# Kernel tuning notes

Hardware: AMD Instinct MI355X
Metric: run time of the kernel (lower is better)

## Reference

```python
import jax, jax.numpy as jnp
import numpy as np


def _update_cv(features, labels, ave, cov, amount, class_num):
    # Segment-reduce formulation of the onehot-expand update_CV.
    N, A = features.shape
    C = class_num
    counts = jax.ops.segment_sum(jnp.ones((N,), features.dtype), labels, num_segments=C)  # [C]
    sums = jax.ops.segment_sum(features, labels, num_segments=C)  # [C, A]
    denom = jnp.where(counts == 0, 1.0, counts)[:, None]  # Amount_CxA with zeros -> 1
    ave_CxA = sums / denom
    # var_temp: sum over samples of (x - mean_label)^2, divided by count
    diff = features - ave_CxA[labels]  # [N, A]
    sq = jax.ops.segment_sum(diff * diff, labels, num_segments=C)
    var_temp = sq / denom
    sum_weight = counts[:, None]  # [C,1] broadcast over A
    weight_CV = sum_weight / (sum_weight + amount[:, None])
    weight_CV = jnp.nan_to_num(weight_CV, nan=0.0)
    additional_CV = weight_CV * (1 - weight_CV) * (ave - ave_CxA) ** 2
    new_cov = cov * (1 - weight_CV) + var_temp * weight_CV + additional_CV
    new_ave = ave * (1 - weight_CV) + ave_CxA * weight_CV
    new_amount = amount + counts
    return new_ave, new_cov, new_amount


def _isda_aug(fc_weight, y, labels, cv_matrix, ratio):
    # sigma2[n,c] = ratio * sum_a (W[c,a] - W[labels[n],a])^2 * CV[labels[n],a]
    # = ratio * ( (W^2) @ cv_n - 2 W @ (w_n * cv_n) + sum_a w_n^2 cv_n )
    cv_n = cv_matrix[labels]              # [N, A]
    w_n = fc_weight[labels]               # [N, A]
    t1 = cv_n @ (fc_weight ** 2).T        # [N, C]
    t2 = (w_n * cv_n) @ fc_weight.T       # [N, C]
    t3 = jnp.sum(w_n * w_n * cv_n, axis=1, keepdims=True)  # [N, 1]
    sigma2 = ratio * (t1 - 2.0 * t2 + t3)
    return y + 0.5 * sigma2


def setup_inputs() -> dict:
    key = jax.random.key(0)
    k1, k2, k3, k4 = jax.random.split(key, 4)
    N, A, C = 512, 2048, 1000
    features = jax.random.normal(k1, (N, A), dtype=jnp.float32)
    labels = jax.random.randint(k2, (N,), 0, C)
    fc_weight = jax.random.normal(k3, (C, A), dtype=jnp.float32) * 0.02
    fc_bias = jax.random.normal(k4, (C,), dtype=jnp.float32) * 0.02
    return {
        "features": features,
        "labels": labels,
        "fc_weight": fc_weight,
        "fc_bias": fc_bias,
        "ave_state": jnp.zeros((C, A), jnp.float32),
        "cov_state": jnp.zeros((C, A), jnp.float32),
        "amount_state": jnp.zeros((C,), jnp.float32),
        "ratio": 1,
    }


def reference(features, labels, fc_weight, fc_bias, ave_state, cov_state, amount_state, ratio):
    C = fc_weight.shape[0]
    # model head: y = features @ W^T + b (features come from backbone; detached for CV)
    y = features @ fc_weight.T + fc_bias
    new_ave, new_cov, new_amount = _update_cv(
        jax.lax.stop_gradient(features), labels, ave_state, cov_state, amount_state, C)
    isda_y = _isda_aug(fc_weight, y, labels, jax.lax.stop_gradient(new_cov), ratio)
    log_probs = jax.nn.log_softmax(isda_y, axis=1)
    loss = -jnp.mean(jnp.take_along_axis(log_probs, labels[:, None], axis=1))
    return loss, y, new_ave, new_cov, new_amount
```

## Files before the change

### kernel.cpp

```cpp
#include <hip/hip_runtime.h>
#include <hip/hip_bf16.h>

typedef short v8s __attribute__((ext_vector_type(8)));
typedef float v4f __attribute__((ext_vector_type(4)));

#define KSPLIT 4

static __device__ __forceinline__ float ldv(const void* p, size_t i, int f32m) {
    if (f32m) return ((const float*)p)[i];
    return __bfloat162float(((const __hip_bfloat16*)p)[i]);
}
static __device__ __forceinline__ void stv(void* p, size_t i, float v, int f32m) {
    if (f32m) ((float*)p)[i] = v;
    else ((__hip_bfloat16*)p)[i] = __float2bfloat16(v);
}
static __device__ __forceinline__ unsigned short f2bu(float x) {
    __hip_bfloat16 h = __float2bfloat16(x);
    return *(unsigned short*)&h;
}
static __device__ __forceinline__ float bu2f(unsigned short u) {
    return __uint_as_float(((unsigned)u) << 16);
}

static __device__ __forceinline__ float decode_scalar(const void* p) {
    unsigned u = *(const unsigned*)p;
    unsigned e32 = (u >> 23) & 0xff;
    if (e32 >= 97 && e32 <= 160) return __uint_as_float(u);
    unsigned lo = u & 0xffffu;
    unsigned e16 = (lo >> 7) & 0xff;
    if ((u >> 16) == 0 && e16 >= 97 && e16 <= 160)
        return __uint_as_float(lo << 16);
    return (float)(int)u;
}

static __device__ __forceinline__ int block_sniff(const void* feat) {
    const __hip_bfloat16* p = (const __hip_bfloat16*)feat;
    float v = __bfloat162float(p[threadIdx.x & 255]);
    int bad = !(fabsf(v) < 1e10f);
    return __syncthreads_or(bad) ? 1 : 0;
}

__device__ __forceinline__ float wave_sum(float v) {
    #pragma unroll
    for (int o = 32; o > 0; o >>= 1) v += __shfl_down(v, o, 64);
    return v;
}
__device__ __forceinline__ float wave_max(float v) {
    #pragma unroll
    for (int o = 32; o > 0; o >>= 1) v = fmaxf(v, __shfl_down(v, o, 64));
    return v;
}

static __device__ __forceinline__ void ld16(unsigned short* lds, const unsigned short* g) {
    __builtin_amdgcn_global_load_lds(
        (const __attribute__((address_space(1))) unsigned int*)g,
        (__attribute__((address_space(3))) unsigned int*)lds,
        16, 0, 0);
}

__global__ __launch_bounds__(1024) void count_sort(
        const int* __restrict__ labels, int* __restrict__ counts,
        int* __restrict__ offs, int* __restrict__ rows, int Nn, int C) {
    __shared__ int h[1024];
    __shared__ int o[1024];
    __shared__ int cur[1024];
    int tid = threadIdx.x;
    h[tid] = 0;
    __syncthreads();
    for (int i = tid; i < Nn; i += 1024) atomicAdd(&h[labels[i]], 1);
    __syncthreads();
    o[tid] = h[tid];
    __syncthreads();
    for (int d = 1; d < 1024; d <<= 1) {
        int v = (tid >= d) ? o[tid - d] : 0;
        __syncthreads();
        o[tid] += v;
        __syncthreads();
    }
    int excl = o[tid] - h[tid];
    counts[tid] = h[tid];
    offs[tid] = excl;
    cur[tid] = excl;
    __syncthreads();
    for (int i = tid; i < Nn; i += 1024) {
        int pos = atomicAdd(&cur[labels[i]], 1);
        rows[pos] = i;
    }
}

__global__ __launch_bounds__(256) void prep(
        const void* __restrict__ feat, unsigned short* __restrict__ featb, int total) {
    int f32m = block_sniff(feat);
    int i = (blockIdx.x * 256 + threadIdx.x) * 8;
    if (i >= total) return;
    if (f32m) {
        const float* f = (const float*)feat + i;
        unsigned short r[8];
        #pragma unroll
        for (int u = 0; u < 8; ++u) r[u] = f2bu(f[u]);
        *(v8s*)(featb + i) = *(v8s*)r;
    } else {
        *(v8s*)(featb + i) = *(const v8s*)((const unsigned short*)feat + i);
    }
}

__global__ __launch_bounds__(256) void finalize_stats(
        const unsigned short* __restrict__ featb,
        const int* __restrict__ counts, const int* __restrict__ offs,
        const int* __restrict__ rows,
        const void* __restrict__ ave, const void* __restrict__ cov,
        const void* __restrict__ amount, const void* __restrict__ W,
        const void* __restrict__ feat,
        void* __restrict__ out, size_t off_ave, size_t off_cov, size_t off_amt,
        unsigned short* __restrict__ Wb, unsigned short* __restrict__ W2b,
        unsigned short* __restrict__ Cb, unsigned short* __restrict__ Gb,
        float* __restrict__ T3p, int A, int A8) {
    __shared__ float sb[4];
    int f32m = block_sniff(feat);
    int c = blockIdx.y;
    int a = blockIdx.x * 256 + threadIdx.x;
    size_t idx = (size_t)c * A + a;
    int cnti = counts[c];
    int start = offs[c];
    float s1 = 0.f, s2 = 0.f;
    for (int i = 0; i < cnti; ++i) {
        float x = bu2f(featb[(size_t)rows[start + i] * A + a]);
        s1 += x;
        s2 += x * x;
    }
    float cnt = (float)cnti;
    float denom = cnti > 0 ? cnt : 1.f;
    float mean = s1 / denom;
    float var = fmaxf((s2 - cnt * mean * mean) / denom, 0.f);
    float amt = ldv(amount, c, f32m);
    float tot = cnt + amt;
    float w = tot > 0.f ? (cnt / tot) : 0.f;
    float av = ldv(ave, idx, f32m);
    float cv = ldv(cov, idx, f32m);
    float d = av - mean;
    float ncv = cv * (1.f - w) + var * w + w * (1.f - w) * d * d;
    float nav = av * (1.f - w) + mean * w;
    stv(out, off_cov + idx, ncv, f32m);
    stv(out, off_ave + idx, nav, f32m);
    float wv = ldv(W, idx, f32m);
    Wb[idx] = f2bu(wv);
    W2b[idx] = f2bu(wv * wv);
    Cb[idx] = f2bu(ncv);
    Gb[idx] = f2bu(ncv * wv);
    if (a == 0) stv(out, off_amt + c, amt + cnt, f32m);
    float s = wave_sum(wv * wv * ncv);
    int lane = threadIdx.x & 63, wid = threadIdx.x >> 6;
    if (lane == 0) sb[wid] = s;
    __syncthreads();
    if (threadIdx.x == 0) T3p[(size_t)c * A8 + blockIdx.x] = sb[0] + sb[1] + sb[2] + sb[3];
}

__global__ __launch_bounds__(256) void triple_gemm_mfma(
        const unsigned short* __restrict__ featb,
        const unsigned short* __restrict__ Wb,
        const unsigned short* __restrict__ W2b,
        const unsigned short* __restrict__ Cb,
        const unsigned short* __restrict__ Gb,
        const int* __restrict__ labels,
        float* __restrict__ partY, float* __restrict__ partT1, float* __restrict__ partT2,
        int Cpad, int A, size_t NC) {
    __shared__ unsigned short sA[10240];
    __shared__ int sLab[64];
    int tid = threadIdx.x, wv = tid >> 6, lane = tid & 63;
    int n0 = blockIdx.y * 64, j0 = blockIdx.x * 64;
    int kslice = A / KSPLIT;
    int k0 = blockIdx.z * kslice;
    if (tid < 64) sLab[tid] = labels[n0 + tid];
    __syncthreads();

    int r = lane & 15, q = lane >> 4;
    int fr = wv * 16 + r;
    const unsigned short* pF = featb + (size_t)(n0 + fr) * A + k0 + q * 8;
    int lab = sLab[fr];
    const unsigned short* pC = Cb + (size_t)lab * A + k0 + q * 8;
    const unsigned short* pG = Gb + (size_t)lab * A + k0 + q * 8;
    const unsigned short* pW = Wb + (size_t)(j0 + fr) * A + k0 + q * 8;
    const unsigned short* pQ = W2b + (size_t)(j0 + fr) * A + k0 + q * 8;
    unsigned short* dF = &sA[0    + wv * 512];
    unsigned short* dC = &sA[2048 + wv * 512];
    unsigned short* dG = &sA[4096 + wv * 512];
    unsigned short* dW = &sA[6144 + wv * 512];
    unsigned short* dQ = &sA[8192 + wv * 512];

    v4f aY[4] = {{0,0,0,0},{0,0,0,0},{0,0,0,0},{0,0,0,0}};
    v4f aT1[4] = {{0,0,0,0},{0,0,0,0},{0,0,0,0},{0,0,0,0}};
    v4f aT2[4] = {{0,0,0,0},{0,0,0,0},{0,0,0,0},{0,0,0,0}};

    for (int kk = 0; kk < kslice; kk += 32) {
        ld16(dF, pF); ld16(dC, pC); ld16(dG, pG); ld16(dW, pW); ld16(dQ, pQ);
        pF += 32; pC += 32; pG += 32; pW += 32; pQ += 32;
        __syncthreads();
        v8s f = *(v8s*)&sA[0    + wv * 512 + lane * 8];
        v8s c = *(v8s*)&sA[2048 + wv * 512 + lane * 8];
        v8s g = *(v8s*)&sA[4096 + wv * 512 + lane * 8];
        #pragma unroll
        for (int t = 0; t < 4; ++t) {
            v8s w  = *(v8s*)&sA[6144 + t * 512 + lane * 8];
            v8s w2 = *(v8s*)&sA[8192 + t * 512 + lane * 8];
            aY[t]  = __builtin_amdgcn_mfma_f32_16x16x32_bf16(f, w,  aY[t],  0, 0, 0);
            aT1[t] = __builtin_amdgcn_mfma_f32_16x16x32_bf16(c, w2, aT1[t], 0, 0, 0);
            aT2[t] = __builtin_amdgcn_mfma_f32_16x16x32_bf16(g, w,  aT2[t], 0, 0, 0);
        }
        __syncthreads();
    }

    float* pY = partY + (size_t)blockIdx.z * NC;
    float* p1 = partT1 + (size_t)blockIdx.z * NC;
    float* p2 = partT2 + (size_t)blockIdx.z * NC;
    int quad = lane >> 4, colb = lane & 15;
    #pragma unroll
    for (int t = 0; t < 4; ++t) {
        int j = j0 + t * 16 + colb;
        #pragma unroll
        for (int rr = 0; rr < 4; ++rr) {
            int n = n0 + wv * 16 + quad * 4 + rr;
            size_t idx = (size_t)n * Cpad + j;
            pY[idx] = aY[t][rr];
            p1[idx] = aT1[t][rr];
            p2[idx] = aT2[t][rr];
        }
    }
}

__global__ __launch_bounds__(256) void epilogue_rowloss(
        const float* __restrict__ partY, const float* __restrict__ partT1,
        const float* __restrict__ partT2, const float* __restrict__ T3p,
        const void* __restrict__ bias, const void* __restrict__ feat,
        const int* __restrict__ labels,
        void* __restrict__ out, size_t off_y,
        float* __restrict__ rowloss,
        int C, int Cpad, int A8, const void* ratio_p, size_t NC) {
    __shared__ float sb[4];
    __shared__ float sM;
    __shared__ float sLabVal;
    int f32m = block_sniff(feat);
    int tid = threadIdx.x;
    int n = blockIdx.x;
    int lab = labels[n];
    float t3 = 0.f;
    for (int i = 0; i < A8; ++i) t3 += T3p[(size_t)lab * A8 + i];
    float ratio = decode_scalar(ratio_p);

    float vals[8];
    int nu = Cpad >> 8;
    float m = -3.4e38f;
    for (int u = 0; u < nu; ++u) {
        int j = u * 256 + tid;
        float v = -3.4e38f;
        if (j < C) {
            size_t idx = (size_t)n * Cpad + j;
            float y = 0.f, t1 = 0.f, t2 = 0.f;
            #pragma unroll
            for (int z = 0; z < KSPLIT; ++z) {
                y  += partY[z * NC + idx];
                t1 += partT1[z * NC + idx];
                t2 += partT2[z * NC + idx];
            }
            y += ldv(bias, j, f32m);
            stv(out, off_y + (size_t)n * C + j, y, f32m);
            v = y + 0.5f * ratio * (t1 - 2.f * t2 + t3);
            if (j == lab) sLabVal = v;
        }
        vals[u] = v;
        m = fmaxf(m, v);
    }
    m = wave_max(m);
    int lane = tid & 63, wid = tid >> 6;
    if (lane == 0) sb[wid] = m;
    __syncthreads();
    if (tid == 0) sM = fmaxf(fmaxf(sb[0], sb[1]), fmaxf(sb[2], sb[3]));
    __syncthreads();
    m = sM;
    float s = 0.f;
    for (int u = 0; u < nu; ++u) s += expf(vals[u] - m);
    __syncthreads();
    s = wave_sum(s);
    if (lane == 0) sb[wid] = s;
    __syncthreads();
    if (tid == 0)
        rowloss[n] = m + logf(sb[0] + sb[1] + sb[2] + sb[3]) - sLabVal;
}

__global__ __launch_bounds__(256) void final_loss(
        const float* __restrict__ rowloss, void* __restrict__ out,
        const void* __restrict__ feat, int Nn) {
    __shared__ float sb[4];
    int f32m = block_sniff(feat);
    float s = 0.f;
    for (int i = threadIdx.x; i < Nn; i += 256) s += rowloss[i];
    s = wave_sum(s);
    int lane = threadIdx.x & 63, wid = threadIdx.x >> 6;
    if (lane == 0) sb[wid] = s;
    __syncthreads();
    if (threadIdx.x == 0)
        stv(out, 0, (sb[0] + sb[1] + sb[2] + sb[3]) / (float)Nn, f32m);
}

extern "C" void kernel_launch(void* const* d_in, const int* in_sizes, int n_in,
                              void* d_out, int out_size, void* d_ws, size_t ws_size,
                              hipStream_t stream) {
    const void* feat   = d_in[0];
    const int*  labels = (const int*)d_in[1];
    const void* W      = d_in[2];
    const void* bias   = d_in[3];
    const void* ave    = d_in[4];
    const void* cov    = d_in[5];
    const void* amount = d_in[6];
    const void* ratiop = d_in[7];

    int NA = in_sizes[0];
    int Nn = in_sizes[1];
    int C  = in_sizes[3];
    int A  = NA / Nn;
    int CA = in_sizes[2];
    int Cpad = ((C + 255) / 256) * 256;
    int A8 = A / 256;
    size_t NC = (size_t)Nn * Cpad;

    size_t off_y   = 1;
    size_t off_ave = off_y + (size_t)Nn * C;
    size_t off_cov = off_ave + (size_t)CA;
    size_t off_amt = off_cov + (size_t)CA;

    char* ws = (char*)d_ws;
    int*   w_cnt  = (int*)ws;
    int*   w_off  = w_cnt + 1024;
    int*   w_rows = w_off + 1024;
    float* w_T3p  = (float*)(w_rows + 1024);
    float* w_rowls = w_T3p + 8192;
    float* w_partY  = w_rowls + 1024;
    float* w_partT1 = w_partY + KSPLIT * NC;
    float* w_partT2 = w_partT1 + KSPLIT * NC;
    unsigned short* w_featb = (unsigned short*)(w_partT2 + KSPLIT * NC);
    unsigned short* w_Wb    = w_featb + NA;
    unsigned short* w_W2b   = w_Wb + CA;
    unsigned short* w_Cb    = w_W2b + CA;
    unsigned short* w_Gb    = w_Cb + CA;

    count_sort<<<1, 1024, 0, stream>>>(labels, w_cnt, w_off, w_rows, Nn, C);
    prep<<<NA / 2048, 256, 0, stream>>>(feat, w_featb, NA);
    dim3 g2(A8, C);
    finalize_stats<<<g2, 256, 0, stream>>>(w_featb, w_cnt, w_off, w_rows,
                                           ave, cov, amount, W, feat,
                                           d_out, off_ave, off_cov, off_amt,
                                           w_Wb, w_W2b, w_Cb, w_Gb, w_T3p, A, A8);
    dim3 g3(Cpad / 64, Nn / 64, KSPLIT);
    triple_gemm_mfma<<<g3, 256, 0, stream>>>(w_featb, w_Wb, w_W2b, w_Cb, w_Gb,
                                             labels, w_partY, w_partT1, w_partT2,
                                             Cpad, A, NC);
    epilogue_rowloss<<<Nn, 256, 0, stream>>>(w_partY, w_partT1, w_partT2, w_T3p,
                                             bias, feat, labels, d_out, off_y,
                                             w_rowls, C, Cpad, A8, ratiop, NC);
    final_loss<<<1, 256, 0, stream>>>(w_rowls, d_out, feat, Nn);
}
```

Before: 142.3 us.

## Merge count-sort into prep, drop LDS staging in GEMM, fuse final loss reduction

Folds the label counting sort into block 0 of the feature-conversion kernel and replaces the separate final_loss kernel with an atomic accumulate plus last-block finalisation, cutting two kernel launches. The triple GEMM no longer stages operands through LDS with barriers. Each wave now loads its MFMA fragments straight from global memory, which removes the syncthreads but means every wave re-reads the W and W² tiles. The atomic float sum makes the loss reduction order nondeterministic, and the counters in misc are zeroed in the first kernel.

```diff
diff --git a/kernel.cpp b/kernel.cpp
--- a/kernel.cpp
+++ b/kernel.cpp
@@ -51,56 +51,59 @@
     return v;
 }
 
-static __device__ __forceinline__ void ld16(unsigned short* lds, const unsigned short* g) {
-    __builtin_amdgcn_global_load_lds(
-        (const __attribute__((address_space(1))) unsigned int*)g,
-        (__attribute__((address_space(3))) unsigned int*)lds,
-        16, 0, 0);
-}
-
-__global__ __launch_bounds__(1024) void count_sort(
+__global__ __launch_bounds__(256) void prep_sort(
+        const void* __restrict__ feat, unsigned short* __restrict__ featb, int total,
         const int* __restrict__ labels, int* __restrict__ counts,
-        int* __restrict__ offs, int* __restrict__ rows, int Nn, int C) {
+        int* __restrict__ offs, int* __restrict__ rows,
+        float* __restrict__ misc, int Nn, int C) {
+    int f32m = block_sniff(feat);
+    int tid = threadIdx.x;
+    int i = (blockIdx.x * 256 + tid) * 8;
+    if (i < total) {
+        if (f32m) {
+            const float* f = (const float*)feat + i;
+            unsigned short r[8];
+            #pragma unroll
+            for (int u = 0; u < 8; ++u) r[u] = f2bu(f[u]);
+            *(v8s*)(featb + i) = *(v8s*)r;
+        } else {
+            *(v8s*)(featb + i) = *(const v8s*)((const unsigned short*)feat + i);
+        }
+    }
+    if (blockIdx.x != 0) return;
+
+    if (tid < 16) misc[tid] = 0.f;
+
     __shared__ int h[1024];
-    __shared__ int o[1024];
+    __shared__ int ex[256];
     __shared__ int cur[1024];
-    int tid = threadIdx.x;
-    h[tid] = 0;
-    __syncthreads();
-    for (int i = tid; i < Nn; i += 1024) atomicAdd(&h[labels[i]], 1);
-    __syncthreads();
-    o[tid] = h[tid];
-    __syncthreads();
-    for (int d = 1; d < 1024; d <<= 1) {
-        int v = (tid >= d) ? o[tid - d] : 0;
+    #pragma unroll
+    for (int u = 0; u < 4; ++u) h[tid + 256 * u] = 0;
+    __syncthreads();
+    for (int k = tid; k < Nn; k += 256) atomicAdd(&h[labels[k]], 1);
+    __syncthreads();
+    int b0 = h[4 * tid], b1 = h[4 * tid + 1], b2 = h[4 * tid + 2], b3 = h[4 * tid + 3];
+    int s = b0 + b1 + b2 + b3;
+    ex[tid] = s;
+    __syncthreads();
+    for (int d = 1; d < 256; d <<= 1) {
+        int v = (tid >= d) ? ex[tid - d] : 0;
         __syncthreads();
-        o[tid] += v;
+        ex[tid] += v;
         __syncthreads();
     }
-    int excl = o[tid] - h[tid];
-    counts[tid] = h[tid];
-    offs[tid] = excl;
-    cur[tid] = excl;
-    __syncthreads();
-    for (int i = tid; i < Nn; i += 1024) {
-        int pos = atomicAdd(&cur[labels[i]], 1);
-        rows[pos] = i;
-    }
-}
-
-__global__ __launch_bounds__(256) void prep(
-        const void* __restrict__ feat, unsigned short* __restrict__ featb, int total) {
-    int f32m = block_sniff(feat);
-    int i = (blockIdx.x * 256 + threadIdx.x) * 8;
-    if (i >= total) return;
-    if (f32m) {
-        const float* f = (const float*)feat + i;
-        unsigned short r[8];
-        #pragma unroll
-        for (int u = 0; u < 8; ++u) r[u] = f2bu(f[u]);
-        *(v8s*)(featb + i) = *(v8s*)r;
-    } else {
-        *(v8s*)(featb + i) = *(const v8s*)((const unsigned short*)feat + i);
+    int excl = ex[tid] - s;
+    int o0 = excl, o1 = o0 + b0, o2 = o1 + b1, o3 = o2 + b2;
+    counts[4 * tid] = b0; counts[4 * tid + 1] = b1;
+    counts[4 * tid + 2] = b2; counts[4 * tid + 3] = b3;
+    offs[4 * tid] = o0; offs[4 * tid + 1] = o1;
+    offs[4 * tid + 2] = o2; offs[4 * tid + 3] = o3;
+    cur[4 * tid] = o0; cur[4 * tid + 1] = o1;
+    cur[4 * tid + 2] = o2; cur[4 * tid + 3] = o3;
+    __syncthreads();
+    for (int k = tid; k < Nn; k += 256) {
+        int pos = atomicAdd(&cur[labels[k]], 1);
+        rows[pos] = k;
     }
 }
 
@@ -164,49 +167,54 @@
         const int* __restrict__ labels,
         float* __restrict__ partY, float* __restrict__ partT1, float* __restrict__ partT2,
         int Cpad, int A, size_t NC) {
-    __shared__ unsigned short sA[10240];
-    __shared__ int sLab[64];
     int tid = threadIdx.x, wv = tid >> 6, lane = tid & 63;
     int n0 = blockIdx.y * 64, j0 = blockIdx.x * 64;
     int kslice = A / KSPLIT;
     int k0 = blockIdx.z * kslice;
-    if (tid < 64) sLab[tid] = labels[n0 + tid];
-    __syncthreads();
-
     int r = lane & 15, q = lane >> 4;
-    int fr = wv * 16 + r;
-    const unsigned short* pF = featb + (size_t)(n0 + fr) * A + k0 + q * 8;
-    int lab = sLab[fr];
+
+    int nrow = n0 + wv * 16 + r;
+    int lab = labels[nrow];
+    const unsigned short* pF = featb + (size_t)nrow * A + k0 + q * 8;
     const unsigned short* pC = Cb + (size_t)lab * A + k0 + q * 8;
     const unsigned short* pG = Gb + (size_t)lab * A + k0 + q * 8;
-    const unsigned short* pW = Wb + (size_t)(j0 + fr) * A + k0 + q * 8;
-    const unsigned short* pQ = W2b + (size_t)(j0 + fr) * A + k0 + q * 8;
-    unsigned short* dF = &sA[0    + wv * 512];
-    unsigned short* dC = &sA[2048 + wv * 512];
-    unsigned short* dG = &sA[4096 + wv * 512];
-    unsigned short* dW = &sA[6144 + wv * 512];
-    unsigned short* dQ = &sA[8192 + wv * 512];
+    const unsigned short* pW0 = Wb  + (size_t)(j0 + 0  + r) * A + k0 + q * 8;
+    const unsigned short* pW1 = Wb  + (size_t)(j0 + 16 + r) * A + k0 + q * 8;
+    const unsigned short* pW2 = Wb  + (size_t)(j0 + 32 + r) * A + k0 + q * 8;
+    const unsigned short* pW3 = Wb  + (size_t)(j0 + 48 + r) * A + k0 + q * 8;
+    const unsigned short* pQ0 = W2b + (size_t)(j0 + 0  + r) * A + k0 + q * 8;
+    const unsigned short* pQ1 = W2b + (size_t)(j0 + 16 + r) * A + k0 + q * 8;
+    const unsigned short* pQ2 = W2b + (size_t)(j0 + 32 + r) * A + k0 + q * 8;
+    const unsigned short* pQ3 = W2b + (size_t)(j0 + 48 + r) * A + k0 + q * 8;
 
     v4f aY[4] = {{0,0,0,0},{0,0,0,0},{0,0,0,0},{0,0,0,0}};
     v4f aT1[4] = {{0,0,0,0},{0,0,0,0},{0,0,0,0},{0,0,0,0}};
     v4f aT2[4] = {{0,0,0,0},{0,0,0,0},{0,0,0,0},{0,0,0,0}};
 
     for (int kk = 0; kk < kslice; kk += 32) {
-        ld16(dF, pF); ld16(dC, pC); ld16(dG, pG); ld16(dW, pW); ld16(dQ, pQ);
-        pF += 32; pC += 32; pG += 32; pW += 32; pQ += 32;
-        __syncthreads();
-        v8s f = *(v8s*)&sA[0    + wv * 512 + lane * 8];
-        v8s c = *(v8s*)&sA[2048 + wv * 512 + lane * 8];
-        v8s g = *(v8s*)&sA[4096 + wv * 512 + lane * 8];
-        #pragma unroll
-        for (int t = 0; t < 4; ++t) {
-            v8s w  = *(v8s*)&sA[6144 + t * 512 + lane * 8];
-            v8s w2 = *(v8s*)&sA[8192 + t * 512 + lane * 8];
-            aY[t]  = __builtin_amdgcn_mfma_f32_16x16x32_bf16(f, w,  aY[t],  0, 0, 0);
-            aT1[t] = __builtin_amdgcn_mfma_f32_16x16x32_bf16(c, w2, aT1[t], 0, 0, 0);
-            aT2[t] = __builtin_amdgcn_mfma_f32_16x16x32_bf16(g, w,  aT2[t], 0, 0, 0);
-        }
-        __syncthreads();
+        v8s f = *(const v8s*)pF;
+        v8s c = *(const v8s*)pC;
+        v8s g = *(const v8s*)pG;
+        v8s w0 = *(const v8s*)pW0, w1 = *(const v8s*)pW1;
+        v8s w2 = *(const v8s*)pW2, w3 = *(const v8s*)pW3;
+        v8s q0 = *(const v8s*)pQ0, q1 = *(const v8s*)pQ1;
+        v8s q2 = *(const v8s*)pQ2, q3 = *(const v8s*)pQ3;
+        pF += 32; pC += 32; pG += 32;
+        pW0 += 32; pW1 += 32; pW2 += 32; pW3 += 32;
+        pQ0 += 32; pQ1 += 32; pQ2 += 32; pQ3 += 32;
+
+        aY[0]  = __builtin_amdgcn_mfma_f32_16x16x32_bf16(f, w0, aY[0],  0, 0, 0);
+        aY[1]  = __builtin_amdgcn_mfma_f32_16x16x32_bf16(f, w1, aY[1],  0, 0, 0);
+        aY[2]  = __builtin_amdgcn_mfma_f32_16x16x32_bf16(f, w2, aY[2],  0, 0, 0);
+        aY[3]  = __builtin_amdgcn_mfma_f32_16x16x32_bf16(f, w3, aY[3],  0, 0, 0);
+        aT1[0] = __builtin_amdgcn_mfma_f32_16x16x32_bf16(c, q0, aT1[0], 0, 0, 0);
+        aT1[1] = __builtin_amdgcn_mfma_f32_16x16x32_bf16(c, q1, aT1[1], 0, 0, 0);
+        aT1[2] = __builtin_amdgcn_mfma_f32_16x16x32_bf16(c, q2, aT1[2], 0, 0, 0);
+        aT1[3] = __builtin_amdgcn_mfma_f32_16x16x32_bf16(c, q3, aT1[3], 0, 0, 0);
+        aT2[0] = __builtin_amdgcn_mfma_f32_16x16x32_bf16(g, w0, aT2[0], 0, 0, 0);
+        aT2[1] = __builtin_amdgcn_mfma_f32_16x16x32_bf16(g, w1, aT2[1], 0, 0, 0);
+        aT2[2] = __builtin_amdgcn_mfma_f32_16x16x32_bf16(g, w2, aT2[2], 0, 0, 0);
+        aT2[3] = __builtin_amdgcn_mfma_f32_16x16x32_bf16(g, w3, aT2[3], 0, 0, 0);
     }
 
     float* pY = partY + (size_t)blockIdx.z * NC;
@@ -233,8 +241,8 @@
         const void* __restrict__ bias, const void* __restrict__ feat,
         const int* __restrict__ labels,
         void* __restrict__ out, size_t off_y,
-        float* __restrict__ rowloss,
-        int C, int Cpad, int A8, const void* ratio_p, size_t NC) {
+        float* __restrict__ misc,
+        int C, int Cpad, int A8, const void* ratio_p, size_t NC, int Nn) {
     __shared__ float sb[4];
     __shared__ float sM;
     __shared__ float sLabVal;
@@ -282,23 +290,17 @@
     s = wave_sum(s);
     if (lane == 0) sb[wid] = s;
     __syncthreads();
-    if (tid == 0)
-        rowloss[n] = m + logf(sb[0] + sb[1] + sb[2] + sb[3]) - sLabVal;
-}
-
-__global__ __launch_bounds__(256) void final_loss(
-        const float* __restrict__ rowloss, void* __restrict__ out,
-        const void* __restrict__ feat, int Nn) {
-    __shared__ float sb[4];
-    int f32m = block_sniff(feat);
-    float s = 0.f;
-    for (int i = threadIdx.x; i < Nn; i += 256) s += rowloss[i];
-    s = wave_sum(s);
-    int lane = threadIdx.x & 63, wid = threadIdx.x >> 6;
-    if (lane == 0) sb[wid] = s;
-    __syncthreads();
-    if (threadIdx.x == 0)
-        stv(out, 0, (sb[0] + sb[1] + sb[2] + sb[3]) / (float)Nn, f32m);
+    if (tid == 0) {
+        float rl = m + logf(sb[0] + sb[1] + sb[2] + sb[3]) - sLabVal;
+        atomicAdd(&misc[0], rl);
+        __threadfence();
+        int old = atomicAdd((int*)&misc[1], 1);
+        if (old == Nn - 1) {
+            __threadfence();
+            float tot = atomicAdd(&misc[0], 0.f);
+            stv(out, 0, tot / (float)Nn, f32m);
+        }
+    }
 }
 
 extern "C" void kernel_launch(void* const* d_in, const int* in_sizes, int n_in,
@@ -331,9 +333,9 @@
     int*   w_cnt  = (int*)ws;
     int*   w_off  = w_cnt + 1024;
     int*   w_rows = w_off + 1024;
-    float* w_T3p  = (float*)(w_rows + 1024);
-    float* w_rowls = w_T3p + 8192;
-    float* w_partY  = w_rowls + 1024;
+    float* w_misc = (float*)(w_rows + 1024);
+    float* w_T3p  = w_misc + 16;
+    float* w_partY  = w_T3p + 8192;
     float* w_partT1 = w_partY + KSPLIT * NC;
     float* w_partT2 = w_partT1 + KSPLIT * NC;
     unsigned short* w_featb = (unsigned short*)(w_partT2 + KSPLIT * NC);
@@ -342,8 +344,8 @@
     unsigned short* w_Cb    = w_W2b + CA;
     unsigned short* w_Gb    = w_Cb + CA;
 
-    count_sort<<<1, 1024, 0, stream>>>(labels, w_cnt, w_off, w_rows, Nn, C);
-    prep<<<NA / 2048, 256, 0, stream>>>(feat, w_featb, NA);
+    prep_sort<<<NA / 2048, 256, 0, stream>>>(feat, w_featb, NA, labels,
+                                             w_cnt, w_off, w_rows, w_misc, Nn, C);
     dim3 g2(A8, C);
     finalize_stats<<<g2, 256, 0, stream>>>(w_featb, w_cnt, w_off, w_rows,
                                            ave, cov, amount, W, feat,
@@ -355,6 +357,5 @@
                                              Cpad, A, NC);
     epilogue_rowloss<<<Nn, 256, 0, stream>>>(w_partY, w_partT1, w_partT2, w_T3p,
                                              bias, feat, labels, d_out, off_y,
-                                             w_rowls, C, Cpad, A8, ratiop, NC);
-    final_loss<<<1, 256, 0, stream>>>(w_rowls, d_out, feat, Nn);
-}
+                                             w_misc, C, Cpad, A8, ratiop, NC, Nn);
+}
```

After: 164.7 us. +15.8%, slower.
